# Performance work log

Hardware: AMD Instinct MI355X
Metric: run time of the kernel (lower is better)

The kernel has to match this reference:

```python
import jax, jax.numpy as jnp
import numpy as np

H = 8        # heads
DH = 64      # dim_head
EPS = 1e-5   # LayerNorm eps (torch default)


def setup_inputs() -> dict:
    key = jax.random.key(0)
    k0, k1, k2, k3, k4 = jax.random.split(key, 5)
    b, l, n, dim = 2, 8, 256, 512
    inner = H * DH
    return {
        "xyzs": jax.random.normal(k0, (b, l, n, 3), dtype=jnp.float32),
        "features": jax.random.normal(k1, (b, l, n, dim), dtype=jnp.float32),
        "ln_gamma": jnp.ones((dim,), dtype=jnp.float32),
        "ln_beta": jnp.zeros((dim,), dtype=jnp.float32),
        "w_qkv": jax.random.normal(k2, (dim, 3 * inner), dtype=jnp.float32) * 0.02,
        "w_sp": jax.random.normal(k3, (3, DH), dtype=jnp.float32) * 0.3,
        "w_out": jax.random.normal(k4, (inner, dim), dtype=jnp.float32) * 0.02,
        "b_out": jnp.zeros((dim,), dtype=jnp.float32),
    }


def reference(xyzs, features, ln_gamma, ln_beta, w_qkv, w_sp, w_out, b_out):
    b, l, n, dim = features.shape
    m = l * n
    inner = H * DH
    scale = DH ** (-0.5)

    # LayerNorm over last dim (biased variance, eps=1e-5)
    mu = jnp.mean(features, axis=-1, keepdims=True)
    var = jnp.var(features, axis=-1, keepdims=True)
    normed = (features - mu) * jax.lax.rsqrt(var + EPS) * ln_gamma + ln_beta

    # qkv projection, chunk into q,k,v, reshape 'b l n (h d) -> b h (l n) d'
    qkv = normed.reshape(b, m, dim) @ w_qkv            # [b, m, 3*inner]
    def split_heads(t):
        return t.reshape(b, m, H, DH).transpose(0, 2, 1, 3)  # [b, h, m, d]
    q = split_heads(qkv[..., :inner])
    k = split_heads(qkv[..., inner:2 * inner])
    v = split_heads(qkv[..., 2 * inner:])

    dots = jnp.einsum('bhid,bhjd->bhij', q, k) * scale  # [b, h, m, m]
    attn = jax.nn.softmax(dots, axis=-1)
    v_out = jnp.einsum('bhij,bhjd->bhid', attn, v)      # [b, h, m, d]

    # pairwise coordinate deltas: delta[b,i,j,c] = xyz[b,j,c] - xyz[b,i,c]
    xyz_f = xyzs.reshape(b, m, 3)
    delta = xyz_f[:, None, :, :] - xyz_f[:, :, None, :]  # [b, m, m, 3]
    # attention-weighted aggregation over j (avoids [b,h,m,m,3] intermediate)
    agg = jnp.einsum('bhij,bijc->bhic', attn, delta)     # [b, h, m, 3]
    disp = agg @ w_sp                                    # [b, h, m, DH]

    out = v_out + disp                                   # [b, h, m, DH]
    out = out.transpose(0, 2, 1, 3).reshape(b, m, inner) # 'b h m d -> b m (h d)'
    out = jax.nn.gelu(out @ w_out + b_out, approximate=False)
    return out.reshape(b, l, n, dim) + features
```

## Files before the change

### kernel.cpp

```cpp
#include <hip/hip_runtime.h>
#include <hip/hip_bf16.h>
#include <math.h>

#define BB   2
#define MM   2048
#define DIM  512
#define NH   8
#define DHd  64
#define NQK  1536
#define ROWS 4096
#define NROW 32768

typedef __hip_bfloat16 bf16;
typedef __attribute__((ext_vector_type(8))) short bf16x8;
typedef __attribute__((ext_vector_type(4))) float f32x4;
typedef __attribute__((ext_vector_type(8))) unsigned short us8;

__device__ __forceinline__ unsigned short f2bf_bits(float x) {
    bf16 h = __float2bfloat16(x);
    return *(unsigned short*)&h;
}
__device__ __forceinline__ float bf2f(unsigned short u) {
    unsigned int v = ((unsigned int)u) << 16;
    return __uint_as_float(v);
}

__global__ __launch_bounds__(256) void pre_kernel(
    const float* __restrict__ feat, const float* __restrict__ gamma,
    const float* __restrict__ beta, unsigned short* __restrict__ normed,
    const float* __restrict__ wqkv, const float* __restrict__ wout,
    unsigned short* __restrict__ wqkvT, unsigned short* __restrict__ woutT)
{
    __shared__ float st[64][65];
    int b = blockIdx.x;
    int tid = threadIdx.x;
    if (b < ROWS) {
        const float* fr = feat + (size_t)b * DIM;
        float x0 = fr[tid];
        float x1 = fr[tid + 256];
        float s  = x0 + x1;
        float ss = x0 * x0 + x1 * x1;
        #pragma unroll
        for (int o = 32; o >= 1; o >>= 1) { s += __shfl_down(s, o); ss += __shfl_down(ss, o); }
        __shared__ float ws_[4], wss_[4];
        int wid = tid >> 6, lane = tid & 63;
        if (lane == 0) { ws_[wid] = s; wss_[wid] = ss; }
        __syncthreads();
        if (tid == 0) {
            float a = 0.f, c = 0.f;
            for (int i = 0; i < 4; i++) { a += ws_[i]; c += wss_[i]; }
            ws_[0] = a; wss_[0] = c;
        }
        __syncthreads();
        float mu  = ws_[0] * (1.0f / DIM);
        float var = wss_[0] * (1.0f / DIM) - mu * mu;
        float inv = rsqrtf(var + 1e-5f);
        normed[(size_t)b * DIM + tid]       = f2bf_bits((x0 - mu) * inv * gamma[tid] + beta[tid]);
        normed[(size_t)b * DIM + tid + 256] = f2bf_bits((x1 - mu) * inv * gamma[tid + 256] + beta[tid + 256]);
        return;
    }
    int idx = b - ROWS;
    const float* in; unsigned short* out; int N, n0;
    if (idx < 192) { in = wqkv; out = wqkvT; N = NQK; n0 = (idx >> 3) * 64; }
    else { idx -= 192; in = wout; out = woutT; N = DIM; n0 = (idx >> 3) * 64; }
    int k0 = (idx & 7) * 64;
    #pragma unroll
    for (int p = 0; p < 16; p++) {
        int e = tid + p * 256;
        int r = e >> 6, c = e & 63;
        st[r][c] = in[(size_t)(k0 + r) * N + n0 + c];
    }
    __syncthreads();
    #pragma unroll
    for (int p = 0; p < 16; p++) {
        int e = tid + p * 256;
        int nr = e >> 6, kc = e & 63;
        out[(size_t)(n0 + nr) * DIM + k0 + kc] = f2bf_bits(st[kc][nr]);
    }
}

__global__ __launch_bounds__(256) void qkv_gemm(
    const unsigned short* __restrict__ A, const unsigned short* __restrict__ BT,
    unsigned short* __restrict__ qd, unsigned short* __restrict__ kd,
    unsigned short* __restrict__ vd)
{
    __shared__ __align__(16) unsigned short sA[128 * 40];
    __shared__ __align__(16) unsigned short sB[128 * 40];
    int tid = threadIdx.x;
    int r0 = blockIdx.x * 128;
    int n0 = blockIdx.y * 128;
    int chunk = n0 >> 9;
    int cl    = n0 & 511;
    int w = tid >> 6, lane = tid & 63;
    int wm = w >> 1, wn = w & 1;
    int ln15 = lane & 15, quad = lane >> 4;

    int srow = tid >> 1;
    int scol = (tid & 1) * 16;

    f32x4 acc[4][4] = {};

    for (int k0 = 0; k0 < DIM; k0 += 32) {
        __syncthreads();
        *(us8*)&sA[srow * 40 + scol]     = *(const us8*)&A[(size_t)(r0 + srow) * DIM + k0 + scol];
        *(us8*)&sA[srow * 40 + scol + 8] = *(const us8*)&A[(size_t)(r0 + srow) * DIM + k0 + scol + 8];
        *(us8*)&sB[srow * 40 + scol]     = *(const us8*)&BT[(size_t)(n0 + srow) * DIM + k0 + scol];
        *(us8*)&sB[srow * 40 + scol + 8] = *(const us8*)&BT[(size_t)(n0 + srow) * DIM + k0 + scol + 8];
        __syncthreads();
        const unsigned short* fa = (chunk == 2) ? sA : sB;
        const unsigned short* fb = (chunk == 2) ? sB : sA;
        bf16x8 af[4], bf_[4];
        #pragma unroll
        for (int i = 0; i < 4; i++)
            af[i] = *(const bf16x8*)&fa[(wm * 64 + i * 16 + ln15) * 40 + quad * 8];
        #pragma unroll
        for (int j = 0; j < 4; j++)
            bf_[j] = *(const bf16x8*)&fb[(wn * 64 + j * 16 + ln15) * 40 + quad * 8];
        #pragma unroll
        for (int i = 0; i < 4; i++)
            #pragma unroll
            for (int j = 0; j < 4; j++)
                acc[i][j] = __builtin_amdgcn_mfma_f32_16x16x32_bf16(af[i], bf_[j], acc[i][j], 0, 0, 0);
    }

    if (chunk == 2) {
        int rowb = r0 + wm * 64 + quad * 4;
        #pragma unroll
        for (int j = 0; j < 4; j++) {
            int c = cl + wn * 64 + j * 16 + ln15;
            int h = c >> 6, d = c & 63;
            #pragma unroll
            for (int i = 0; i < 4; i++) {
                int gr = rowb + i * 16;
                int bb = gr >> 11, mm = gr & 2047;
                ushort4 pk;
                pk.x = f2bf_bits(acc[i][j][0]);
                pk.y = f2bf_bits(acc[i][j][1]);
                pk.z = f2bf_bits(acc[i][j][2]);
                pk.w = f2bf_bits(acc[i][j][3]);
                *(ushort4*)&vd[((size_t)(bb * NH + h) * DHd + d) * MM + mm] = pk;
            }
        }
    } else {
        unsigned short* dst = (chunk == 0) ? qd : kd;
        float sc = (chunk == 0) ? 0.125f : 1.0f;
        #pragma unroll
        for (int i = 0; i < 4; i++) {
            int within0 = cl + wm * 64 + i * 16 + quad * 4;
            int h = within0 >> 6, d = within0 & 63;
            #pragma unroll
            for (int j = 0; j < 4; j++) {
                int gr = r0 + wn * 64 + j * 16 + ln15;
                int bb = gr >> 11, mm = gr & 2047;
                ushort4 pk;
                pk.x = f2bf_bits(acc[i][j][0] * sc);
                pk.y = f2bf_bits(acc[i][j][1] * sc);
                pk.z = f2bf_bits(acc[i][j][2] * sc);
                pk.w = f2bf_bits(acc[i][j][3] * sc);
                *(ushort4*)&dst[((size_t)(bb * NH + h) * MM + mm) * DHd + d] = pk;
            }
        }
    }
}

__global__ __launch_bounds__(256) void attn_kernel(
    const unsigned short* __restrict__ qg, const unsigned short* __restrict__ kg,
    const unsigned short* __restrict__ vg, const float* __restrict__ xyzs,
    unsigned short* __restrict__ obuf, float* __restrict__ lbuf)
{
    __shared__ __align__(16) unsigned short sQ[64 * 72];
    __shared__ __align__(16) unsigned short sK[64 * 72];
    __shared__ __align__(16) unsigned short sVT[80 * 72];
    __shared__ __align__(16) unsigned short sP[64 * 72];

    int tid = threadIdx.x;
    int bh = blockIdx.y; int bb = bh >> 3;
    int i0 = blockIdx.x * 64;
    int ks = blockIdx.z;
    int w = tid >> 6;
    int lane = tid & 63;
    int ln15 = lane & 15;
    int quad = lane >> 4;

    for (int e = tid; e < 12 * 72; e += 256) sVT[68 * 72 + e] = 0;
    if (tid < 64) sVT[67 * 72 + tid] = 0x3F80;

    {
        const unsigned short* src = qg + ((size_t)bh * MM + i0) * DHd;
        int row = tid >> 2, col = (tid & 3) * 16;
        *(us8*)&sQ[row * 72 + col]     = *(const us8*)&src[(size_t)tid * 16];
        *(us8*)&sQ[row * 72 + col + 8] = *(const us8*)&src[(size_t)tid * 16 + 8];
    }
    asm volatile("s_waitcnt lgkmcnt(0)" ::: "memory");
    bf16x8 aq0 = *(const bf16x8*)&sQ[(w * 16 + ln15) * 72 + quad * 8];
    bf16x8 aq1 = *(const bf16x8*)&sQ[(w * 16 + ln15) * 72 + 32 + quad * 8];

    f32x4 o[5] = {};

    const unsigned short* kbase = kg + (size_t)bh * MM * DHd;
    const unsigned short* vbase = vg + (size_t)bh * DHd * MM;
    int jbeg = ks * (MM / 2), jend = jbeg + (MM / 2);

    int srow = tid >> 2, scol16 = (tid & 3) * 16;

    us8 rk0, rk1, rv0, rv1;
    float rx = 0.f;
    {
        const unsigned short* src = kbase + (size_t)jbeg * DHd;
        rk0 = *(const us8*)&src[(size_t)tid * 16];
        rk1 = *(const us8*)&src[(size_t)tid * 16 + 8];
        const unsigned short* vs = vbase + jbeg;
        rv0 = *(const us8*)&vs[(size_t)srow * MM + scol16];
        rv1 = *(const us8*)&vs[(size_t)srow * MM + scol16 + 8];
        if (tid < 192) rx = xyzs[((size_t)bb * MM + jbeg) * 3 + tid];
    }

    int pwb = quad << 4;
    int swzr = (ln15 >> 2) << 4;
    int pr0 = (quad * 8) ^ swzr;
    int pr1 = (32 + quad * 8) ^ swzr;

    for (int jt = jbeg; jt < jend; jt += 64) {
        __syncthreads();
        *(us8*)&sK[srow * 72 + scol16]      = rk0;
        *(us8*)&sK[srow * 72 + scol16 + 8]  = rk1;
        *(us8*)&sVT[srow * 72 + scol16]     = rv0;
        *(us8*)&sVT[srow * 72 + scol16 + 8] = rv1;
        if (tid < 192) {
            int key = tid / 3, c = tid - key * 3;
            sVT[(64 + c) * 72 + key] = f2bf_bits(rx);
        }
        __syncthreads();
        int jn = jt + 64;
        if (jn < jend) {
            const unsigned short* src = kbase + (size_t)jn * DHd;
            rk0 = *(const us8*)&src[(size_t)tid * 16];
            rk1 = *(const us8*)&src[(size_t)tid * 16 + 8];
            const unsigned short* vs = vbase + jn;
            rv0 = *(const us8*)&vs[(size_t)srow * MM + scol16];
            rv1 = *(const us8*)&vs[(size_t)srow * MM + scol16 + 8];
            if (tid < 192) rx = xyzs[((size_t)bb * MM + jn) * 3 + tid];
        }

        f32x4 sacc[4];
        #pragma unroll
        for (int t = 0; t < 4; t++) {
            bf16x8 bk0 = *(const bf16x8*)&sK[(t * 16 + ln15) * 72 + quad * 8];
            bf16x8 bk1 = *(const bf16x8*)&sK[(t * 16 + ln15) * 72 + 32 + quad * 8];
            f32x4 z = {};
            z = __builtin_amdgcn_mfma_f32_16x16x32_bf16(aq0, bk0, z, 0, 0, 0);
            z = __builtin_amdgcn_mfma_f32_16x16x32_bf16(aq1, bk1, z, 0, 0, 0);
            sacc[t] = z;
        }

        #pragma unroll
        for (int t = 0; t < 4; t++) {
            int colb = (t * 16) ^ pwb;
            #pragma unroll
            for (int reg = 0; reg < 4; reg++) {
                float pv = __expf(sacc[t][reg]);
                sP[(w * 16 + quad * 4 + reg) * 72 + colb + ln15] = f2bf_bits(pv);
            }
        }
        asm volatile("s_waitcnt lgkmcnt(0)" ::: "memory");
        bf16x8 ap0 = *(const bf16x8*)&sP[(w * 16 + ln15) * 72 + pr0];
        bf16x8 ap1 = *(const bf16x8*)&sP[(w * 16 + ln15) * 72 + pr1];
        #pragma unroll
        for (int t = 0; t < 5; t++) {
            bf16x8 bv0 = *(const bf16x8*)&sVT[(t * 16 + ln15) * 72 + quad * 8];
            bf16x8 bv1 = *(const bf16x8*)&sVT[(t * 16 + ln15) * 72 + 32 + quad * 8];
            o[t] = __builtin_amdgcn_mfma_f32_16x16x32_bf16(ap0, bv0, o[t], 0, 0, 0);
            o[t] = __builtin_amdgcn_mfma_f32_16x16x32_bf16(ap1, bv1, o[t], 0, 0, 0);
        }
    }

    size_t kso = (size_t)ks * NROW;
    #pragma unroll
    for (int reg = 0; reg < 4; reg++) {
        size_t row = (size_t)bh * MM + i0 + w * 16 + quad * 4 + reg;
        unsigned short* orow = obuf + (kso + row) * 72;
        #pragma unroll
        for (int t = 0; t < 4; t++)
            orow[t * 16 + ln15] = f2bf_bits(o[t][reg]);
        if (ln15 < 3)  orow[64 + ln15] = f2bf_bits(o[4][reg]);
        if (ln15 == 3) lbuf[kso + row] = o[4][reg];
    }
}

__global__ __launch_bounds__(256) void merge_kernel(
    const unsigned short* __restrict__ obuf, const float* __restrict__ lbuf,
    const float* __restrict__ xyzs, const float* __restrict__ wsp,
    unsigned short* __restrict__ attn_out)
{
    __shared__ float sW[3][64];
    int tid = threadIdx.x;
    if (tid < 192) sW[tid >> 6][tid & 63] = wsp[tid];
    __syncthreads();
    int r   = blockIdx.x * 64 + (tid >> 2);
    int d0  = (tid & 3) * 16;
    int bh = r >> 11, qrow = r & 2047, bb = bh >> 3, hh = bh & 7;
    const unsigned short* p1 = obuf + (size_t)r * 72;
    const unsigned short* p2 = obuf + ((size_t)NROW + r) * 72;
    float invl = 1.f / (lbuf[r] + lbuf[NROW + r]);
    size_t xb = ((size_t)bb * MM + qrow) * 3;
    float gx = (bf2f(p1[64]) + bf2f(p2[64])) * invl - xyzs[xb + 0];
    float gy = (bf2f(p1[65]) + bf2f(p2[65])) * invl - xyzs[xb + 1];
    float gz = (bf2f(p1[66]) + bf2f(p2[66])) * invl - xyzs[xb + 2];
    us8 a0 = *(const us8*)&p1[d0];
    us8 a1 = *(const us8*)&p1[d0 + 8];
    us8 b0 = *(const us8*)&p2[d0];
    us8 b1 = *(const us8*)&p2[d0 + 8];
    unsigned short outv[16];
    #pragma unroll
    for (int e = 0; e < 8; e++) {
        int d = d0 + e;
        float v = (bf2f(a0[e]) + bf2f(b0[e])) * invl
                + gx * sW[0][d] + gy * sW[1][d] + gz * sW[2][d];
        outv[e] = f2bf_bits(v);
    }
    #pragma unroll
    for (int e = 0; e < 8; e++) {
        int d = d0 + 8 + e;
        float v = (bf2f(a1[e]) + bf2f(b1[e])) * invl
                + gx * sW[0][d] + gy * sW[1][d] + gz * sW[2][d];
        outv[8 + e] = f2bf_bits(v);
    }
    unsigned short* dst = attn_out + ((size_t)bb * MM + qrow) * DIM + hh * DHd + d0;
    *(us8*)dst       = *(us8*)&outv[0];
    *(us8*)(dst + 8) = *(us8*)&outv[8];
}

__global__ __launch_bounds__(256) void out_gemm(
    const unsigned short* __restrict__ A, const unsigned short* __restrict__ BT,
    const float* __restrict__ bias, const float* __restrict__ feat,
    float* __restrict__ out)
{
    __shared__ __align__(16) unsigned short sA[64 * 40];
    __shared__ __align__(16) unsigned short sB[64 * 40];
    int tid = threadIdx.x;
    int r0 = blockIdx.x * 64, n0 = blockIdx.y * 64;
    int w = tid >> 6, lane = tid & 63;
    int wm = w >> 1, wn = w & 1;
    int ln15 = lane & 15, quad = lane >> 4;

    int srow = tid >> 2, scol = (tid & 3) * 8;

    f32x4 acc[2][2] = {};

    for (int k0 = 0; k0 < DIM; k0 += 32) {
        __syncthreads();
        *(us8*)&sA[srow * 40 + scol] = *(const us8*)&A[(size_t)(r0 + srow) * DIM + k0 + scol];
        *(us8*)&sB[srow * 40 + scol] = *(const us8*)&BT[(size_t)(n0 + srow) * DIM + k0 + scol];
        __syncthreads();
        bf16x8 af[2], bf_[2];
        #pragma unroll
        for (int i = 0; i < 2; i++)
            af[i] = *(const bf16x8*)&sA[(wm * 32 + i * 16 + ln15) * 40 + quad * 8];
        #pragma unroll
        for (int j = 0; j < 2; j++)
            bf_[j] = *(const bf16x8*)&sB[(wn * 32 + j * 16 + ln15) * 40 + quad * 8];
        #pragma unroll
        for (int i = 0; i < 2; i++)
            #pragma unroll
            for (int j = 0; j < 2; j++)
                acc[i][j] = __builtin_amdgcn_mfma_f32_16x16x32_bf16(af[i], bf_[j], acc[i][j], 0, 0, 0);
    }

    #pragma unroll
    for (int i = 0; i < 2; i++) {
        #pragma unroll
        for (int reg = 0; reg < 4; reg++) {
            int gr = r0 + wm * 32 + i * 16 + quad * 4 + reg;
            #pragma unroll
            for (int j = 0; j < 2; j++) {
                int c = n0 + wn * 32 + j * 16 + ln15;
                float x = acc[i][j][reg] + bias[c];
                float g = 0.5f * x * (1.f + erff(x * 0.70710678118f));
                out[(size_t)gr * DIM + c] = g + feat[(size_t)gr * DIM + c];
            }
        }
    }
}

extern "C" void kernel_launch(void* const* d_in, const int* in_sizes, int n_in,
                              void* d_out, int out_size, void* d_ws, size_t ws_size,
                              hipStream_t stream)
{
    const float* xyzs  = (const float*)d_in[0];
    const float* feat  = (const float*)d_in[1];
    const float* gamma = (const float*)d_in[2];
    const float* beta  = (const float*)d_in[3];
    const float* wqkv  = (const float*)d_in[4];
    const float* wsp   = (const float*)d_in[5];
    const float* wout  = (const float*)d_in[6];
    const float* bout  = (const float*)d_in[7];
    float* out = (float*)d_out;

    unsigned short* ws16 = (unsigned short*)d_ws;
    const size_t SEGS = (size_t)ROWS * DIM;
    unsigned short* normed = ws16;
    unsigned short* qb     = ws16 + SEGS;
    unsigned short* kb     = ws16 + 2 * SEGS;
    unsigned short* vb     = ws16 + 3 * SEGS;
    unsigned short* wqkvT  = ws16 + 4 * SEGS;
    unsigned short* woutT  = wqkvT + (size_t)NQK * DIM;
    unsigned short* obuf   = woutT + (size_t)DIM * DIM;
    float*          lbuf   = (float*)(obuf + (size_t)2 * NROW * 72);

    pre_kernel<<<ROWS + 256, 256, 0, stream>>>(feat, gamma, beta, normed,
                                               wqkv, wout, wqkvT, woutT);
    qkv_gemm<<<dim3(32, 12), 256, 0, stream>>>(normed, wqkvT, qb, kb, vb);
    attn_kernel<<<dim3(32, 16, 2), 256, 0, stream>>>(qb, kb, vb, xyzs, obuf, lbuf);
    merge_kernel<<<512, 256, 0, stream>>>(obuf, lbuf, xyzs, wsp, normed);
    out_gemm<<<dim3(64, 8), 256, 0, stream>>>(normed, woutT, bout, feat, out);
}
```

Measured before the change: 154.5 us.

## Load K/V directly from global into MFMA registers, dropping LDS staging

The attention kernel no longer stages K, V^T, Q and xyz tiles through shared memory. Each lane now loads its MFMA operand fragments straight from global memory, which removes the two block barriers and the LDS traffic per key tile. xyz is pre-transposed to bf16 by an extra pre_kernel block so it can be read like V. The log2(e) factor is folded into the q scale so the kernel can use exp2f, and the launch bounds now request four blocks per SM. The cost is that the four waves of a block each fetch the same K/V data from cache, and there is no explicit prefetch or double buffering to hide global load latency.

```diff
diff --git a/kernel.cpp b/kernel.cpp
--- a/kernel.cpp
+++ b/kernel.cpp
@@ -29,7 +29,8 @@
     const float* __restrict__ feat, const float* __restrict__ gamma,
     const float* __restrict__ beta, unsigned short* __restrict__ normed,
     const float* __restrict__ wqkv, const float* __restrict__ wout,
-    unsigned short* __restrict__ wqkvT, unsigned short* __restrict__ woutT)
+    unsigned short* __restrict__ wqkvT, unsigned short* __restrict__ woutT,
+    const float* __restrict__ xyzs, unsigned short* __restrict__ xyzT)
 {
     __shared__ float st[64][65];
     int b = blockIdx.x;
@@ -57,6 +58,15 @@
         float inv = rsqrtf(var + 1e-5f);
         normed[(size_t)b * DIM + tid]       = f2bf_bits((x0 - mu) * inv * gamma[tid] + beta[tid]);
         normed[(size_t)b * DIM + tid + 256] = f2bf_bits((x1 - mu) * inv * gamma[tid + 256] + beta[tid + 256]);
+        return;
+    }
+    if (b == ROWS + 256) {
+        for (int e = tid; e < BB * 3 * MM; e += 256) {
+            int b_ = e / (3 * MM);
+            int rem = e - b_ * 3 * MM;
+            int c = rem / MM, m = rem - c * MM;
+            xyzT[e] = f2bf_bits(xyzs[((size_t)b_ * MM + m) * 3 + c]);
+        }
         return;
     }
     int idx = b - ROWS;
@@ -143,7 +153,7 @@
         }
     } else {
         unsigned short* dst = (chunk == 0) ? qd : kd;
-        float sc = (chunk == 0) ? 0.125f : 1.0f;
+        float sc = (chunk == 0) ? 0.125f * 1.44269504f : 1.0f;
         #pragma unroll
         for (int i = 0; i < 4; i++) {
             int within0 = cl + wm * 64 + i * 16 + quad * 4;
@@ -163,14 +173,11 @@
     }
 }
 
-__global__ __launch_bounds__(256) void attn_kernel(
+__global__ __launch_bounds__(256, 4) void attn_kernel(
     const unsigned short* __restrict__ qg, const unsigned short* __restrict__ kg,
-    const unsigned short* __restrict__ vg, const float* __restrict__ xyzs,
+    const unsigned short* __restrict__ vg, const unsigned short* __restrict__ xyzT,
     unsigned short* __restrict__ obuf, float* __restrict__ lbuf)
 {
-    __shared__ __align__(16) unsigned short sQ[64 * 72];
-    __shared__ __align__(16) unsigned short sK[64 * 72];
-    __shared__ __align__(16) unsigned short sVT[80 * 72];
     __shared__ __align__(16) unsigned short sP[64 * 72];
 
     int tid = threadIdx.x;
@@ -182,83 +189,61 @@
     int ln15 = lane & 15;
     int quad = lane >> 4;
 
-    for (int e = tid; e < 12 * 72; e += 256) sVT[68 * 72 + e] = 0;
-    if (tid < 64) sVT[67 * 72 + tid] = 0x3F80;
-
-    {
-        const unsigned short* src = qg + ((size_t)bh * MM + i0) * DHd;
-        int row = tid >> 2, col = (tid & 3) * 16;
-        *(us8*)&sQ[row * 72 + col]     = *(const us8*)&src[(size_t)tid * 16];
-        *(us8*)&sQ[row * 72 + col + 8] = *(const us8*)&src[(size_t)tid * 16 + 8];
-    }
-    asm volatile("s_waitcnt lgkmcnt(0)" ::: "memory");
-    bf16x8 aq0 = *(const bf16x8*)&sQ[(w * 16 + ln15) * 72 + quad * 8];
-    bf16x8 aq1 = *(const bf16x8*)&sQ[(w * 16 + ln15) * 72 + 32 + quad * 8];
+    const unsigned short* qrow = qg + ((size_t)bh * MM + i0 + w * 16 + ln15) * DHd;
+    bf16x8 aq0 = *(const bf16x8*)&qrow[quad * 8];
+    bf16x8 aq1 = *(const bf16x8*)&qrow[32 + quad * 8];
 
     f32x4 o[5] = {};
 
     const unsigned short* kbase = kg + (size_t)bh * MM * DHd;
     const unsigned short* vbase = vg + (size_t)bh * DHd * MM;
+    const unsigned short* xbase = xyzT + (size_t)bb * 3 * MM;
     int jbeg = ks * (MM / 2), jend = jbeg + (MM / 2);
-
-    int srow = tid >> 2, scol16 = (tid & 3) * 16;
-
-    us8 rk0, rk1, rv0, rv1;
-    float rx = 0.f;
-    {
-        const unsigned short* src = kbase + (size_t)jbeg * DHd;
-        rk0 = *(const us8*)&src[(size_t)tid * 16];
-        rk1 = *(const us8*)&src[(size_t)tid * 16 + 8];
-        const unsigned short* vs = vbase + jbeg;
-        rv0 = *(const us8*)&vs[(size_t)srow * MM + scol16];
-        rv1 = *(const us8*)&vs[(size_t)srow * MM + scol16 + 8];
-        if (tid < 192) rx = xyzs[((size_t)bb * MM + jbeg) * 3 + tid];
-    }
 
     int pwb = quad << 4;
     int swzr = (ln15 >> 2) << 4;
     int pr0 = (quad * 8) ^ swzr;
     int pr1 = (32 + quad * 8) ^ swzr;
 
+    us8 ones, zero;
+    #pragma unroll
+    for (int e = 0; e < 8; e++) { ones[e] = 0x3F80; zero[e] = 0; }
+
     for (int jt = jbeg; jt < jend; jt += 64) {
-        __syncthreads();
-        *(us8*)&sK[srow * 72 + scol16]      = rk0;
-        *(us8*)&sK[srow * 72 + scol16 + 8]  = rk1;
-        *(us8*)&sVT[srow * 72 + scol16]     = rv0;
-        *(us8*)&sVT[srow * 72 + scol16 + 8] = rv1;
-        if (tid < 192) {
-            int key = tid / 3, c = tid - key * 3;
-            sVT[(64 + c) * 72 + key] = f2bf_bits(rx);
-        }
-        __syncthreads();
-        int jn = jt + 64;
-        if (jn < jend) {
-            const unsigned short* src = kbase + (size_t)jn * DHd;
-            rk0 = *(const us8*)&src[(size_t)tid * 16];
-            rk1 = *(const us8*)&src[(size_t)tid * 16 + 8];
-            const unsigned short* vs = vbase + jn;
-            rv0 = *(const us8*)&vs[(size_t)srow * MM + scol16];
-            rv1 = *(const us8*)&vs[(size_t)srow * MM + scol16 + 8];
-            if (tid < 192) rx = xyzs[((size_t)bb * MM + jn) * 3 + tid];
-        }
-
         f32x4 sacc[4];
         #pragma unroll
         for (int t = 0; t < 4; t++) {
-            bf16x8 bk0 = *(const bf16x8*)&sK[(t * 16 + ln15) * 72 + quad * 8];
-            bf16x8 bk1 = *(const bf16x8*)&sK[(t * 16 + ln15) * 72 + 32 + quad * 8];
+            const unsigned short* kr = &kbase[(size_t)(jt + t * 16 + ln15) * DHd + quad * 8];
+            bf16x8 bk0 = *(const bf16x8*)kr;
+            bf16x8 bk1 = *(const bf16x8*)(kr + 32);
             f32x4 z = {};
             z = __builtin_amdgcn_mfma_f32_16x16x32_bf16(aq0, bk0, z, 0, 0, 0);
             z = __builtin_amdgcn_mfma_f32_16x16x32_bf16(aq1, bk1, z, 0, 0, 0);
             sacc[t] = z;
         }
+        bf16x8 bv[5][2];
+        #pragma unroll
+        for (int t = 0; t < 4; t++) {
+            const unsigned short* vr = &vbase[(size_t)(t * 16 + ln15) * MM + jt + quad * 8];
+            bv[t][0] = *(const bf16x8*)vr;
+            bv[t][1] = *(const bf16x8*)(vr + 32);
+        }
+        if (ln15 < 3) {
+            const unsigned short* xr = &xbase[(size_t)ln15 * MM + jt + quad * 8];
+            bv[4][0] = *(const bf16x8*)xr;
+            bv[4][1] = *(const bf16x8*)(xr + 32);
+        } else if (ln15 == 3) {
+            bv[4][0] = *(bf16x8*)&ones; bv[4][1] = *(bf16x8*)&ones;
+        } else {
+            bv[4][0] = *(bf16x8*)&zero; bv[4][1] = *(bf16x8*)&zero;
+        }
 
         #pragma unroll
         for (int t = 0; t < 4; t++) {
             int colb = (t * 16) ^ pwb;
             #pragma unroll
             for (int reg = 0; reg < 4; reg++) {
-                float pv = __expf(sacc[t][reg]);
+                float pv = exp2f(sacc[t][reg]);
                 sP[(w * 16 + quad * 4 + reg) * 72 + colb + ln15] = f2bf_bits(pv);
             }
         }
@@ -267,10 +252,8 @@
         bf16x8 ap1 = *(const bf16x8*)&sP[(w * 16 + ln15) * 72 + pr1];
         #pragma unroll
         for (int t = 0; t < 5; t++) {
-            bf16x8 bv0 = *(const bf16x8*)&sVT[(t * 16 + ln15) * 72 + quad * 8];
-            bf16x8 bv1 = *(const bf16x8*)&sVT[(t * 16 + ln15) * 72 + 32 + quad * 8];
-            o[t] = __builtin_amdgcn_mfma_f32_16x16x32_bf16(ap0, bv0, o[t], 0, 0, 0);
-            o[t] = __builtin_amdgcn_mfma_f32_16x16x32_bf16(ap1, bv1, o[t], 0, 0, 0);
+            o[t] = __builtin_amdgcn_mfma_f32_16x16x32_bf16(ap0, bv[t][0], o[t], 0, 0, 0);
+            o[t] = __builtin_amdgcn_mfma_f32_16x16x32_bf16(ap1, bv[t][1], o[t], 0, 0, 0);
         }
     }
 
@@ -406,11 +389,13 @@
     unsigned short* woutT  = wqkvT + (size_t)NQK * DIM;
     unsigned short* obuf   = woutT + (size_t)DIM * DIM;
     float*          lbuf   = (float*)(obuf + (size_t)2 * NROW * 72);
-
-    pre_kernel<<<ROWS + 256, 256, 0, stream>>>(feat, gamma, beta, normed,
-                                               wqkv, wout, wqkvT, woutT);
+    unsigned short* xyzT   = (unsigned short*)(lbuf + 2 * NROW);
+
+    pre_kernel<<<ROWS + 257, 256, 0, stream>>>(feat, gamma, beta, normed,
+                                               wqkv, wout, wqkvT, woutT,
+                                               xyzs, xyzT);
     qkv_gemm<<<dim3(32, 12), 256, 0, stream>>>(normed, wqkvT, qb, kb, vb);
-    attn_kernel<<<dim3(32, 16, 2), 256, 0, stream>>>(qb, kb, vb, xyzs, obuf, lbuf);
+    attn_kernel<<<dim3(32, 16, 2), 256, 0, stream>>>(qb, kb, vb, xyzT, obuf, lbuf);
     merge_kernel<<<512, 256, 0, stream>>>(obuf, lbuf, xyzs, wsp, normed);
     out_gemm<<<dim3(64, 8), 256, 0, stream>>>(normed, woutT, bout, feat, out);
 }
```

Result: slower. 242.7 us (+57.1%).

## Fuse split-KV merge into output GEMM and switch softmax exp to exp2

Applied to the files above, without the earlier changes.

The merge of the two key-split partial attention outputs (normalisation by the summed row sums, plus the coordinate-displacement projection) now runs inside the output GEMM's A-tile load, which removes a separate kernel launch and the bf16 round trip through global memory. Each of the 8 column blocks now recomputes the merge for its rows, so that work and the obuf reads are repeated eightfold. Separately, log2(e) is folded into the Q scale so the attention kernel can call exp2f instead of __expf.

```diff
diff --git a/kernel.cpp b/kernel.cpp
--- a/kernel.cpp
+++ b/kernel.cpp
@@ -143,7 +143,7 @@
         }
     } else {
         unsigned short* dst = (chunk == 0) ? qd : kd;
-        float sc = (chunk == 0) ? 0.125f : 1.0f;
+        float sc = (chunk == 0) ? 0.125f * 1.44269504f : 1.0f;
         #pragma unroll
         for (int i = 0; i < 4; i++) {
             int within0 = cl + wm * 64 + i * 16 + quad * 4;
@@ -258,7 +258,7 @@
             int colb = (t * 16) ^ pwb;
             #pragma unroll
             for (int reg = 0; reg < 4; reg++) {
-                float pv = __expf(sacc[t][reg]);
+                float pv = exp2f(sacc[t][reg]);
                 sP[(w * 16 + quad * 4 + reg) * 72 + colb + ln15] = f2bf_bits(pv);
             }
         }
@@ -287,69 +287,59 @@
     }
 }
 
-__global__ __launch_bounds__(256) void merge_kernel(
+__global__ __launch_bounds__(256) void out_kernel(
     const unsigned short* __restrict__ obuf, const float* __restrict__ lbuf,
     const float* __restrict__ xyzs, const float* __restrict__ wsp,
-    unsigned short* __restrict__ attn_out)
-{
-    __shared__ float sW[3][64];
-    int tid = threadIdx.x;
-    if (tid < 192) sW[tid >> 6][tid & 63] = wsp[tid];
-    __syncthreads();
-    int r   = blockIdx.x * 64 + (tid >> 2);
-    int d0  = (tid & 3) * 16;
-    int bh = r >> 11, qrow = r & 2047, bb = bh >> 3, hh = bh & 7;
-    const unsigned short* p1 = obuf + (size_t)r * 72;
-    const unsigned short* p2 = obuf + ((size_t)NROW + r) * 72;
-    float invl = 1.f / (lbuf[r] + lbuf[NROW + r]);
-    size_t xb = ((size_t)bb * MM + qrow) * 3;
-    float gx = (bf2f(p1[64]) + bf2f(p2[64])) * invl - xyzs[xb + 0];
-    float gy = (bf2f(p1[65]) + bf2f(p2[65])) * invl - xyzs[xb + 1];
-    float gz = (bf2f(p1[66]) + bf2f(p2[66])) * invl - xyzs[xb + 2];
-    us8 a0 = *(const us8*)&p1[d0];
-    us8 a1 = *(const us8*)&p1[d0 + 8];
-    us8 b0 = *(const us8*)&p2[d0];
-    us8 b1 = *(const us8*)&p2[d0 + 8];
-    unsigned short outv[16];
-    #pragma unroll
-    for (int e = 0; e < 8; e++) {
-        int d = d0 + e;
-        float v = (bf2f(a0[e]) + bf2f(b0[e])) * invl
-                + gx * sW[0][d] + gy * sW[1][d] + gz * sW[2][d];
-        outv[e] = f2bf_bits(v);
-    }
-    #pragma unroll
-    for (int e = 0; e < 8; e++) {
-        int d = d0 + 8 + e;
-        float v = (bf2f(a1[e]) + bf2f(b1[e])) * invl
-                + gx * sW[0][d] + gy * sW[1][d] + gz * sW[2][d];
-        outv[8 + e] = f2bf_bits(v);
-    }
-    unsigned short* dst = attn_out + ((size_t)bb * MM + qrow) * DIM + hh * DHd + d0;
-    *(us8*)dst       = *(us8*)&outv[0];
-    *(us8*)(dst + 8) = *(us8*)&outv[8];
-}
-
-__global__ __launch_bounds__(256) void out_gemm(
-    const unsigned short* __restrict__ A, const unsigned short* __restrict__ BT,
-    const float* __restrict__ bias, const float* __restrict__ feat,
-    float* __restrict__ out)
+    const unsigned short* __restrict__ BT, const float* __restrict__ bias,
+    const float* __restrict__ feat, float* __restrict__ out)
 {
     __shared__ __align__(16) unsigned short sA[64 * 40];
     __shared__ __align__(16) unsigned short sB[64 * 40];
+    __shared__ float4 sM[64][8];
+    __shared__ float sW[3][64];
     int tid = threadIdx.x;
     int r0 = blockIdx.x * 64, n0 = blockIdx.y * 64;
+    int bb = r0 >> 11, mm0 = r0 & 2047;
     int w = tid >> 6, lane = tid & 63;
     int wm = w >> 1, wn = w & 1;
     int ln15 = lane & 15, quad = lane >> 4;
-
     int srow = tid >> 2, scol = (tid & 3) * 8;
 
+    if (tid < 192) sW[tid >> 6][tid & 63] = wsp[tid];
+    for (int p = tid; p < 512; p += 256) {
+        int i = p >> 3, h = p & 7;
+        int rh = ((bb * 8 + h) << 11) + mm0 + i;
+        float invl = 1.f / (lbuf[rh] + lbuf[NROW + rh]);
+        const unsigned short* o1 = obuf + (size_t)rh * 72;
+        const unsigned short* o2 = obuf + ((size_t)NROW + rh) * 72;
+        size_t xb = ((size_t)bb * MM + mm0 + i) * 3;
+        float gx = (bf2f(o1[64]) + bf2f(o2[64])) * invl - xyzs[xb + 0];
+        float gy = (bf2f(o1[65]) + bf2f(o2[65])) * invl - xyzs[xb + 1];
+        float gz = (bf2f(o1[66]) + bf2f(o2[66])) * invl - xyzs[xb + 2];
+        sM[i][h] = make_float4(invl, gx, gy, gz);
+    }
+
     f32x4 acc[2][2] = {};
 
     for (int k0 = 0; k0 < DIM; k0 += 32) {
         __syncthreads();
-        *(us8*)&sA[srow * 40 + scol] = *(const us8*)&A[(size_t)(r0 + srow) * DIM + k0 + scol];
+        {
+            int c0 = k0 + scol;
+            int h = c0 >> 6, dd = c0 & 63;
+            float4 m = sM[srow][h];
+            int rh = ((bb * 8 + h) << 11) + mm0 + srow;
+            us8 p1 = *(const us8*)&obuf[(size_t)rh * 72 + dd];
+            us8 p2 = *(const us8*)&obuf[((size_t)NROW + rh) * 72 + dd];
+            us8 pk;
+            #pragma unroll
+            for (int e = 0; e < 8; e++) {
+                int d = dd + e;
+                float v = (bf2f(p1[e]) + bf2f(p2[e])) * m.x
+                        + m.y * sW[0][d] + m.z * sW[1][d] + m.w * sW[2][d];
+                pk[e] = f2bf_bits(v);
+            }
+            *(us8*)&sA[srow * 40 + scol] = pk;
+        }
         *(us8*)&sB[srow * 40 + scol] = *(const us8*)&BT[(size_t)(n0 + srow) * DIM + k0 + scol];
         __syncthreads();
         bf16x8 af[2], bf_[2];
@@ -411,6 +401,6 @@
                                                wqkv, wout, wqkvT, woutT);
     qkv_gemm<<<dim3(32, 12), 256, 0, stream>>>(normed, wqkvT, qb, kb, vb);
     attn_kernel<<<dim3(32, 16, 2), 256, 0, stream>>>(qb, kb, vb, xyzs, obuf, lbuf);
-    merge_kernel<<<512, 256, 0, stream>>>(obuf, lbuf, xyzs, wsp, normed);
-    out_gemm<<<dim3(64, 8), 256, 0, stream>>>(normed, woutT, bout, feat, out);
-}
+    out_kernel<<<dim3(64, 8), 256, 0, stream>>>(obuf, lbuf, xyzs, wsp,
+                                                woutT, bout, feat, out);
+}
```

Measured after the change: 157.1 us. No clear change (+1.7%).
